# Kernel tuning notes

Hardware: AMD Instinct MI355X
Metric: run time of the kernel (lower is better)

The kernel has to match this reference:

```python
import jax, jax.numpy as jnp
import numpy as np

NEG_SLOPE = 0.2
N_NODES = 50000
N_EDGES = 800000
IN_DIM = 256
HID_DIM = 256
HEADS = 8
HEAD_DIM = HID_DIM // HEADS


def setup_inputs() -> dict:
    key = jax.random.key(0)
    ks = jax.random.split(key, 12)
    def glorot(k, shape):
        fan = sum(shape[-2:]) if len(shape) > 1 else shape[-1] + 1
        return jax.random.normal(k, shape, jnp.float32) * jnp.sqrt(2.0 / fan)
    return {
        "data": jax.random.normal(ks[0], (N_NODES, IN_DIM), jnp.float32),
        "src": jax.random.randint(ks[1], (N_EDGES,), 0, N_NODES),
        "dst": jax.random.randint(ks[2], (N_EDGES,), 0, N_NODES),
        "W1": glorot(ks[3], (IN_DIM, HID_DIM)),
        "al1": glorot(ks[4], (HEADS, HEAD_DIM)),
        "ar1": glorot(ks[5], (HEADS, HEAD_DIM)),
        "b1": jnp.zeros((HID_DIM,), jnp.float32),
        "W2": glorot(ks[6], (HID_DIM, HID_DIM)),
        "al2": glorot(ks[7], (HEADS, HEAD_DIM)),
        "ar2": glorot(ks[8], (HEADS, HEAD_DIM)),
        "b2": jnp.zeros((HID_DIM,), jnp.float32),
    }


def gat_layer(x, src, dst, W, al, ar, b):
    """One DGL-style GATConv layer with ReLU activation."""
    N = x.shape[0]
    feat = (x @ W).reshape(N, HEADS, HEAD_DIM)            # [N,H,D]
    el = jnp.sum(feat * al[None], axis=-1)                # [N,H]
    er = jnp.sum(feat * ar[None], axis=-1)                # [N,H]
    e = el[src] + er[dst]                                  # [E,H]
    e = jnp.where(e > 0, e, NEG_SLOPE * e)                 # LeakyReLU(0.2)
    # segment softmax over incoming edges of each dst node
    m = jax.ops.segment_max(e, dst, num_segments=N)        # [N,H] (-inf for empty)
    a = jnp.exp(e - m[dst])                                # [E,H]
    denom = jax.ops.segment_sum(a, dst, num_segments=N)    # [N,H]
    alpha = a / denom[dst]                                 # [E,H]
    msg = feat[src] * alpha[:, :, None]                    # [E,H,D]
    out = jax.ops.segment_sum(msg, dst, num_segments=N)    # [N,H,D]
    out = out + b.reshape(1, HEADS, HEAD_DIM)
    out = jax.nn.relu(out)
    return out.reshape(N, HID_DIM)


def reference(data, src, dst, W1, al1, ar1, b1, W2, al2, ar2, b2):
    h = gat_layer(data, src, dst, W1, al1, ar1, b1)
    h = gat_layer(h, src, dst, W2, al2, ar2, b2)
    return h
```

## Files before the change

### kernel.cpp

```cpp
#include <hip/hip_runtime.h>

#define N_NODES 50000
#define N_EDGES 800000
#define DIM 256
#define HEADS 8
#define NEG_SLOPE 0.2f

typedef unsigned short u16;
typedef float floatx4 __attribute__((ext_vector_type(4)));
typedef __bf16 bf16x8 __attribute__((ext_vector_type(8)));

__device__ __forceinline__ float b2f(u16 u) {
    union { unsigned int i; float f; } v; v.i = ((unsigned int)u) << 16; return v.f;
}
__device__ __forceinline__ u16 f2b(float f) {
    union { float f; unsigned int i; } v; v.f = f;
    unsigned int x = v.i;
    if ((x & 0x7f800000u) == 0x7f800000u && (x & 0x007fffffu)) {
        return (u16)((x >> 16) | 0x0040u);
    }
    unsigned int r = (x + 0x7fffu + ((x >> 16) & 1u)) >> 16;
    return (u16)r;
}

__global__ __launch_bounds__(256) void fill_u32(unsigned int* __restrict__ p,
                                                unsigned int v, int n) {
    int i = blockIdx.x * 256 + threadIdx.x;
    if (i < n) p[i] = v;
}

__global__ __launch_bounds__(256) void init_kernel(const unsigned int* __restrict__ d,
                                                   int* __restrict__ counts,
                                                   int* __restrict__ flag) {
    int i = blockIdx.x * 256 + threadIdx.x;
    if (i < N_NODES) counts[i] = 0;
    if (blockIdx.x == 0) {
        __shared__ int cnt;
        if (threadIdx.x == 0) cnt = 0;
        __syncthreads();
        unsigned int w = d[threadIdx.x];
        int bad = 0;
        #pragma unroll
        for (int half = 0; half < 2; ++half) {
            u16 u = (u16)(w >> (16 * half));
            unsigned int e = (u >> 7) & 0xFFu;
            if (u != 0 && (e >= 141u || e <= 27u)) bad = 1;
        }
        atomicAdd(&cnt, bad);
        __syncthreads();
        if (threadIdx.x == 0) *flag = (cnt > 64) ? 1 : 0;
    }
}

__global__ __launch_bounds__(256) void prep_kernel(const void* __restrict__ W1,
                                                   const void* __restrict__ W2,
                                                   u16* __restrict__ Wt1,
                                                   u16* __restrict__ Wt2,
                                                   const int* __restrict__ flagp) {
    const int isf = *flagp;
    int b = blockIdx.x;
    const void* W = (b < 16) ? W1 : W2;
    u16* Wt = (b < 16) ? Wt1 : Wt2;
    int t = b & 15;
    int k0 = (t >> 2) * 64, n0 = (t & 3) * 64;
    __shared__ float lt[64][65];
    int c = threadIdx.x & 63, r0 = threadIdx.x >> 6;
    #pragma unroll
    for (int j = 0; j < 16; ++j) {
        int r = j * 4 + r0;
        lt[r][c] = isf ? ((const float*)W)[(k0 + r) * 256 + n0 + c]
                       : b2f(((const u16*)W)[(k0 + r) * 256 + n0 + c]);
    }
    __syncthreads();
    #pragma unroll
    for (int j = 0; j < 16; ++j) {
        int rn = j * 4 + r0;
        Wt[(n0 + rn) * 256 + k0 + c] = f2b(lt[c][rn]);
    }
}

__global__ __launch_bounds__(256) void hist_kernel(const int* __restrict__ dst,
                                                   int* __restrict__ counts, int E) {
    int i = blockIdx.x * 256 + threadIdx.x;
    if (i < E) atomicAdd(&counts[dst[i]], 1);
}

__global__ __launch_bounds__(256) void scan_partial(const int* __restrict__ counts,
                                                    int* __restrict__ partial, int n) {
    int b = blockIdx.x, tid = threadIdx.x;
    int base = b * 1024 + tid * 4;
    int s = 0;
    #pragma unroll
    for (int k = 0; k < 4; ++k) if (base + k < n) s += counts[base + k];
    int lane = tid & 63;
    #pragma unroll
    for (int off = 32; off; off >>= 1) s += __shfl_xor(s, off);
    __shared__ int wsum[4];
    if (lane == 0) wsum[tid >> 6] = s;
    __syncthreads();
    if (tid == 0) partial[b] = wsum[0] + wsum[1] + wsum[2] + wsum[3];
}

__global__ __launch_bounds__(64) void scan_offsets(const int* __restrict__ partial,
                                                   int* __restrict__ offsets,
                                                   int* __restrict__ row_ptr,
                                                   int nb, int n) {
    int t = threadIdx.x;
    int v0 = (t < nb) ? partial[t] : 0;
    int v = v0;
    #pragma unroll
    for (int d = 1; d < 64; d <<= 1) {
        int u = __shfl_up(v, d);
        if (t >= d) v += u;
    }
    if (t < nb) offsets[t] = v - v0;
    if (t == 63) row_ptr[n] = v;
}

__global__ __launch_bounds__(256) void scan_write(const int* __restrict__ counts,
                                                  const int* __restrict__ offsets,
                                                  int* __restrict__ row_ptr,
                                                  int* __restrict__ wptr, int n) {
    int b = blockIdx.x, tid = threadIdx.x;
    int base = b * 1024 + tid * 4;
    int v[4]; int s = 0;
    #pragma unroll
    for (int k = 0; k < 4; ++k) { v[k] = (base + k < n) ? counts[base + k] : 0; s += v[k]; }
    int lane = tid & 63, w = tid >> 6;
    int incl = s;
    #pragma unroll
    for (int d = 1; d < 64; d <<= 1) {
        int u = __shfl_up(incl, d);
        if (lane >= d) incl += u;
    }
    __shared__ int wsum[4];
    if (lane == 63) wsum[w] = incl;
    __syncthreads();
    int woff = 0;
    for (int i = 0; i < w; ++i) woff += wsum[i];
    int run = offsets[b] + woff + incl - s;
    #pragma unroll
    for (int k = 0; k < 4; ++k) {
        if (base + k < n) { row_ptr[base + k] = run; wptr[base + k] = run; run += v[k]; }
    }
}

__global__ __launch_bounds__(256) void scatter_kernel(const int* __restrict__ src,
                                                      const int* __restrict__ dst,
                                                      int* __restrict__ wptr,
                                                      int* __restrict__ src_sorted, int E) {
    int i = blockIdx.x * 256 + threadIdx.x;
    if (i < E) {
        int pos = atomicAdd(&wptr[dst[i]], 1);
        src_sorted[pos] = src[i];
    }
}

#define LDA 264

__global__ __launch_bounds__(256, 3) void gemm_fused(const void* __restrict__ Araw,
                                                     int maybe_f32,
                                                     const u16* __restrict__ Wt,
                                                     u16* __restrict__ outF,
                                                     float* __restrict__ el,
                                                     float* __restrict__ er,
                                                     const void* __restrict__ al,
                                                     const void* __restrict__ ar,
                                                     int M, const int* __restrict__ flagp) {
    const int isf = *flagp;
    const bool af32 = (maybe_f32 != 0) && (isf != 0);
    __shared__ u16 As[64][LDA];
    const int tid  = threadIdx.x;
    const int w    = tid >> 6;
    const int lane = tid & 63;
    const int quad = lane >> 4;
    const int l16  = lane & 15;
    const int m0   = blockIdx.x * 64;

    const u16* wbase = Wt + (size_t)(64 * w + l16) * 256 + quad * 8;

    bf16x8 bCur[4], bNxt[4], aCur[4], aNxt[4];
    #pragma unroll
    for (int t = 0; t < 4; ++t)
        bCur[t] = *(const bf16x8*)(wbase + (size_t)t * 16 * 256);

    if (af32) {
        const float* Af = (const float*)Araw;
        #pragma unroll
        for (int it = 0; it < 8; ++it) {
            int idx = it * 256 + tid;
            int r = idx >> 5;
            int c = (idx & 31) << 3;
            int gr = m0 + r;
            u16 tb[8];
            if (gr < M) {
                float4 f0 = *(const float4*)(Af + (size_t)gr * 256 + c);
                float4 f1 = *(const float4*)(Af + (size_t)gr * 256 + c + 4);
                tb[0] = f2b(f0.x); tb[1] = f2b(f0.y); tb[2] = f2b(f0.z); tb[3] = f2b(f0.w);
                tb[4] = f2b(f1.x); tb[5] = f2b(f1.y); tb[6] = f2b(f1.z); tb[7] = f2b(f1.w);
            } else {
                #pragma unroll
                for (int k = 0; k < 8; ++k) tb[k] = 0;
            }
            *(uint4*)&As[r][c] = *(uint4*)tb;
        }
    } else {
        const u16* Ab = (const u16*)Araw;
        #pragma unroll
        for (int it = 0; it < 8; ++it) {
            int idx = it * 256 + tid;
            int r = idx >> 5;
            int c = (idx & 31) << 3;
            int gr = m0 + r;
            if (gr < M) {
                *(uint4*)&As[r][c] = *(const uint4*)(Ab + (size_t)gr * 256 + c);
            } else {
                uint4 z = {0u, 0u, 0u, 0u};
                *(uint4*)&As[r][c] = z;
            }
        }
    }
    __syncthreads();

    #pragma unroll
    for (int i = 0; i < 4; ++i)
        aCur[i] = *(const bf16x8*)&As[16 * i + l16][quad * 8];

    floatx4 acc[4][4] = {};

    #pragma unroll
    for (int s = 0; s < 8; ++s) {
        if (s < 7) {
            #pragma unroll
            for (int t = 0; t < 4; ++t)
                bNxt[t] = *(const bf16x8*)(wbase + (size_t)t * 16 * 256 + (s + 1) * 32);
            #pragma unroll
            for (int i = 0; i < 4; ++i)
                aNxt[i] = *(const bf16x8*)&As[16 * i + l16][(s + 1) * 32 + quad * 8];
        }
        #pragma unroll
        for (int i = 0; i < 4; ++i)
            #pragma unroll
            for (int t = 0; t < 4; ++t)
                acc[i][t] = __builtin_amdgcn_mfma_f32_16x16x32_bf16(aCur[i], bCur[t], acc[i][t], 0, 0, 0);
        if (s < 7) {
            #pragma unroll
            for (int t = 0; t < 4; ++t) bCur[t] = bNxt[t];
            #pragma unroll
            for (int i = 0; i < 4; ++i) aCur[i] = aNxt[i];
        }
    }

    #pragma unroll
    for (int i = 0; i < 4; ++i)
        #pragma unroll
        for (int t = 0; t < 4; ++t)
            #pragma unroll
            for (int r = 0; r < 4; ++r) {
                int row = m0 + 16 * i + quad * 4 + r;
                if (row < M) outF[(size_t)row * 256 + 64 * w + 16 * t + l16] = f2b(acc[i][t][r]);
            }

    float alv[4], arv[4];
    #pragma unroll
    for (int t = 0; t < 4; ++t) {
        int c = 64 * w + 16 * t + l16;
        alv[t] = isf ? ((const float*)al)[c] : b2f(((const u16*)al)[c]);
        arv[t] = isf ? ((const float*)ar)[c] : b2f(((const u16*)ar)[c]);
    }
    #pragma unroll
    for (int i = 0; i < 4; ++i)
        #pragma unroll
        for (int r = 0; r < 4; ++r) {
            int row = m0 + 16 * i + quad * 4 + r;
            #pragma unroll
            for (int tt = 0; tt < 2; ++tt) {
                float pl = acc[i][2 * tt][r] * alv[2 * tt] + acc[i][2 * tt + 1][r] * alv[2 * tt + 1];
                float pr = acc[i][2 * tt][r] * arv[2 * tt] + acc[i][2 * tt + 1][r] * arv[2 * tt + 1];
                #pragma unroll
                for (int mask = 1; mask <= 8; mask <<= 1) {
                    pl += __shfl_xor(pl, mask);
                    pr += __shfl_xor(pr, mask);
                }
                if (l16 == 0 && row < M) {
                    el[row * 8 + 2 * w + tt] = pl;
                    er[row * 8 + 2 * w + tt] = pr;
                }
            }
        }
}

__global__ __launch_bounds__(256) void aggregate_kernel(const u16* __restrict__ feat,
                                                        const float* __restrict__ el,
                                                        const float* __restrict__ er,
                                                        const void* __restrict__ bias,
                                                        const int* __restrict__ row_ptr,
                                                        const int* __restrict__ src_sorted,
                                                        void* __restrict__ out,
                                                        int out_mode,
                                                        int node0,
                                                        const int* __restrict__ flagp) {
    const int isf = *flagp;
    const int lane = threadIdx.x & 63;
    const int node = node0 + blockIdx.x * 4 + (threadIdx.x >> 6);
    if (node >= N_NODES) return;
    const int h = lane >> 3;
    const int j = lane & 7;
    const int beg = row_ptr[node];
    const int deg = row_ptr[node + 1] - beg;
    const float ern = er[node * HEADS + h];

    float m0v = -1e30f, ss0 = 0.f;
    float m1v = -1e30f, ss1 = 0.f;
    for (int i = j; i < deg; i += 16) {
        int s0 = src_sorted[beg + i];
        int i2 = i + 8;
        int s1 = (i2 < deg) ? src_sorted[beg + i2] : 0;
        float e0 = el[s0 * 8 + h] + ern;
        float e1 = el[s1 * 8 + h] + ern;
        e0 = e0 > 0.f ? e0 : NEG_SLOPE * e0;
        e1 = e1 > 0.f ? e1 : NEG_SLOPE * e1;
        if (i2 >= deg) e1 = -3e30f;
        float mn0 = fmaxf(m0v, e0);
        ss0 = ss0 * __expf(m0v - mn0) + __expf(e0 - mn0);
        m0v = mn0;
        float mn1 = fmaxf(m1v, e1);
        ss1 = ss1 * __expf(m1v - mn1) + __expf(e1 - mn1);
        m1v = mn1;
    }
    float m = fmaxf(m0v, m1v);
    float ssum = ss0 * __expf(m0v - m) + ss1 * __expf(m1v - m);
    #pragma unroll
    for (int mask = 1; mask <= 4; mask <<= 1) {
        float mo = __shfl_xor(m, mask);
        float so = __shfl_xor(ssum, mask);
        float mn = fmaxf(m, mo);
        ssum = ssum * __expf(m - mn) + so * __expf(mo - mn);
        m = mn;
    }
    const float mx = m;
    const float inv = ssum > 0.f ? 1.f / ssum : 0.f;

    const int q = lane & 31;
    const int half = lane >> 5;
    const int hq = q >> 2;
    float a[8] = {};

    int sC = 0; float avC = 0.f;
    if (j < deg) {
        sC = src_sorted[beg + j];
        float e = el[sC * 8 + h] + ern;
        e = e > 0.f ? e : NEG_SLOPE * e;
        avC = __expf(e - mx) * inv;
    }
    uint4 f[4]; float ae[4];
    #pragma unroll
    for (int u = 0; u < 4; ++u) {
        int sel = hq * 8 + 2 * u + half;
        int se = __shfl(sC, sel);
        ae[u] = __shfl(avC, sel);
        f[u] = *(const uint4*)(feat + (size_t)se * DIM + 8 * q);
    }

    #pragma unroll 2
    for (int c0 = 0; c0 < deg; c0 += 8) {
        uint4 f2[4]; float ae2[4];
        {
            int sN = 0; float avN = 0.f;
            int i = c0 + 8 + j;
            if (i < deg) {
                sN = src_sorted[beg + i];
                float e = el[sN * 8 + h] + ern;
                e = e > 0.f ? e : NEG_SLOPE * e;
                avN = __expf(e - mx) * inv;
            }
            #pragma unroll
            for (int u = 0; u < 4; ++u) {
                int sel = hq * 8 + 2 * u + half;
                int se = __shfl(sN, sel);
                ae2[u] = __shfl(avN, sel);
                f2[u] = *(const uint4*)(feat + (size_t)se * DIM + 8 * q);
            }
        }
        #pragma unroll
        for (int u = 0; u < 4; ++u) {
            float wgt = ae[u];
            a[0] += wgt * b2f((u16)(f[u].x & 0xffffu)); a[1] += wgt * b2f((u16)(f[u].x >> 16));
            a[2] += wgt * b2f((u16)(f[u].y & 0xffffu)); a[3] += wgt * b2f((u16)(f[u].y >> 16));
            a[4] += wgt * b2f((u16)(f[u].z & 0xffffu)); a[5] += wgt * b2f((u16)(f[u].z >> 16));
            a[6] += wgt * b2f((u16)(f[u].w & 0xffffu)); a[7] += wgt * b2f((u16)(f[u].w >> 16));
        }
        #pragma unroll
        for (int u = 0; u < 4; ++u) { f[u] = f2[u]; ae[u] = ae2[u]; }
    }

    #pragma unroll
    for (int k = 0; k < 8; ++k) a[k] += __shfl_xor(a[k], 32);

    if (half == 0) {
        float o[8];
        if (isf) {
            float4 b0 = *(const float4*)((const float*)bias + 8 * q);
            float4 b1 = *(const float4*)((const float*)bias + 8 * q + 4);
            o[0] = a[0] + b0.x; o[1] = a[1] + b0.y; o[2] = a[2] + b0.z; o[3] = a[3] + b0.w;
            o[4] = a[4] + b1.x; o[5] = a[5] + b1.y; o[6] = a[6] + b1.z; o[7] = a[7] + b1.w;
        } else {
            uint4 bu = *(const uint4*)((const u16*)bias + 8 * q);
            o[0] = a[0] + b2f((u16)(bu.x & 0xffffu)); o[1] = a[1] + b2f((u16)(bu.x >> 16));
            o[2] = a[2] + b2f((u16)(bu.y & 0xffffu)); o[3] = a[3] + b2f((u16)(bu.y >> 16));
            o[4] = a[4] + b2f((u16)(bu.z & 0xffffu)); o[5] = a[5] + b2f((u16)(bu.z >> 16));
            o[6] = a[6] + b2f((u16)(bu.w & 0xffffu)); o[7] = a[7] + b2f((u16)(bu.w >> 16));
        }
        #pragma unroll
        for (int k = 0; k < 8; ++k) o[k] = fmaxf(o[k], 0.f);
        if (out_mode == 0 || !isf) {
            u16 pk[8] = {f2b(o[0]), f2b(o[1]), f2b(o[2]), f2b(o[3]),
                         f2b(o[4]), f2b(o[5]), f2b(o[6]), f2b(o[7])};
            *(uint4*)((u16*)out + (size_t)node * DIM + 8 * q) = *(uint4*)pk;
        } else {
            float4 v0 = {o[0], o[1], o[2], o[3]};
            float4 v1 = {o[4], o[5], o[6], o[7]};
            *(float4*)((float*)out + (size_t)node * DIM + 8 * q) = v0;
            *(float4*)((float*)out + (size_t)node * DIM + 8 * q + 4) = v1;
        }
    }
}

extern "C" void kernel_launch(void* const* d_in, const int* in_sizes, int n_in,
                              void* d_out, int out_size, void* d_ws, size_t ws_size,
                              hipStream_t stream) {
    const void* data = d_in[0];
    const int* src = (const int*)d_in[1];
    const int* dst = (const int*)d_in[2];
    const void* W1  = d_in[3];
    const void* al1 = d_in[4];
    const void* ar1 = d_in[5];
    const void* b1  = d_in[6];
    const void* W2  = d_in[7];
    const void* al2 = d_in[8];
    const void* ar2 = d_in[9];
    const void* b2  = d_in[10];

    const size_t NEEDED =
        (size_t)N_NODES * DIM * 2 +
        (size_t)N_NODES * HEADS * 4 * 2 +
        (size_t)N_NODES * 4 * 2 +
        (size_t)(N_NODES + 4) * 4 +
        (size_t)N_EDGES * 4 +
        2 * 256 * 256 * 2 +
        1024;

    if (ws_size < NEEDED) {
        int nwords = (out_size + 1) / 2;
        fill_u32<<<(nwords + 255) / 256, 256, 0, stream>>>(
            (unsigned int*)d_out, 0x42C842C8u, nwords);
        return;
    }

    char* ws = (char*)d_ws;
    u16* feat = (u16*)ws;        ws += (size_t)N_NODES * DIM * 2;
    float* el = (float*)ws;      ws += (size_t)N_NODES * HEADS * 4;
    float* er = (float*)ws;      ws += (size_t)N_NODES * HEADS * 4;
    int* counts = (int*)ws;      ws += (size_t)N_NODES * 4;
    int* wptr = (int*)ws;        ws += (size_t)N_NODES * 4;
    int* row_ptr = (int*)ws;     ws += (size_t)(N_NODES + 4) * 4;
    int* src_sorted = (int*)ws;  ws += (size_t)N_EDGES * 4;
    u16* Wt1 = (u16*)ws;         ws += 256 * 256 * 2;
    u16* Wt2 = (u16*)ws;         ws += 256 * 256 * 2;
    int* partial = (int*)ws;     ws += 256;
    int* offsets = (int*)ws;     ws += 256;
    int* flag = (int*)ws;        ws += 256;

    u16* h1 = (u16*)d_out;

    const int nb = (N_NODES + 1023) / 1024;

    init_kernel<<<(N_NODES + 255) / 256, 256, 0, stream>>>(
        (const unsigned int*)data, counts, flag);
    prep_kernel<<<32, 256, 0, stream>>>(W1, W2, Wt1, Wt2, flag);
    hist_kernel<<<(N_EDGES + 255) / 256, 256, 0, stream>>>(dst, counts, N_EDGES);
    scan_partial<<<nb, 256, 0, stream>>>(counts, partial, N_NODES);
    scan_offsets<<<1, 64, 0, stream>>>(partial, offsets, row_ptr, nb, N_NODES);
    scan_write<<<nb, 256, 0, stream>>>(counts, offsets, row_ptr, wptr, N_NODES);
    scatter_kernel<<<(N_EDGES + 255) / 256, 256, 0, stream>>>(src, dst, wptr, src_sorted, N_EDGES);

    const int gemm_blocks = (N_NODES + 63) / 64;
    const int HALF = 25000;
    const int agg_half_blocks = HALF / 4;

    gemm_fused<<<gemm_blocks, 256, 0, stream>>>(data, 1, Wt1, feat,
                                                el, er, al1, ar1, N_NODES, flag);
    aggregate_kernel<<<agg_half_blocks, 256, 0, stream>>>(feat, el, er, b1, row_ptr, src_sorted,
                                                          (void*)h1, 0, 0, flag);
    aggregate_kernel<<<agg_half_blocks, 256, 0, stream>>>(feat, el, er, b1, row_ptr, src_sorted,
                                                          (void*)h1, 0, HALF, flag);
    gemm_fused<<<gemm_blocks, 256, 0, stream>>>(h1, 0, Wt2, feat,
                                                el, er, al2, ar2, N_NODES, flag);
    aggregate_kernel<<<agg_half_blocks, 256, 0, stream>>>(feat, el, er, b2, row_ptr, src_sorted,
                                                          d_out, 2, 0, flag);
    aggregate_kernel<<<agg_half_blocks, 256, 0, stream>>>(feat, el, er, b2, row_ptr, src_sorted,
                                                          d_out, 2, HALF, flag);
}
```

Before: 426.8 us.

## Replace CSR build with padded per-node adjacency and stage GEMM output via LDS

Replaces the histogram/scan/scatter CSR construction with a single atomic build kernel that writes each edge into a fixed MAXDEG=64 slot per destination node, sending overflow edges to a global list. The aggregate kernels scan that list only for nodes whose degree exceeds the cap. The GEMM epilogue now stages bf16 results through shared memory so it can issue coalesced 16-byte row stores. This removes four small launches and the scan passes, at the cost of a larger workspace and a slow path for high-degree nodes.

New measurement: 394.4 us. -7.6%, faster.

```diff
diff --git a/kernel.cpp b/kernel.cpp
--- a/kernel.cpp
+++ b/kernel.cpp
@@ -5,6 +5,8 @@
 #define DIM 256
 #define HEADS 8
 #define NEG_SLOPE 0.2f
+#define MAXDEG 64
+#define OVFCAP 65536
 
 typedef unsigned short u16;
 typedef float floatx4 __attribute__((ext_vector_type(4)));
@@ -31,12 +33,13 @@
 
 __global__ __launch_bounds__(256) void init_kernel(const unsigned int* __restrict__ d,
                                                    int* __restrict__ counts,
-                                                   int* __restrict__ flag) {
+                                                   int* __restrict__ flag,
+                                                   int* __restrict__ novf) {
     int i = blockIdx.x * 256 + threadIdx.x;
     if (i < N_NODES) counts[i] = 0;
     if (blockIdx.x == 0) {
         __shared__ int cnt;
-        if (threadIdx.x == 0) cnt = 0;
+        if (threadIdx.x == 0) { cnt = 0; *novf = 0; }
         __syncthreads();
         unsigned int w = d[threadIdx.x];
         int bad = 0;
@@ -76,6 +79,26 @@
     for (int j = 0; j < 16; ++j) {
         int rn = j * 4 + r0;
         Wt[(n0 + rn) * 256 + k0 + c] = f2b(lt[c][rn]);
+    }
+}
+
+__global__ __launch_bounds__(256) void build_kernel(const int* __restrict__ src,
+                                                    const int* __restrict__ dst,
+                                                    int* __restrict__ counts,
+                                                    int* __restrict__ padded,
+                                                    int* __restrict__ novf,
+                                                    int2* __restrict__ ovf, int E) {
+    int i = blockIdx.x * 256 + threadIdx.x;
+    if (i < E) {
+        int d = dst[i];
+        int s = src[i];
+        int pos = atomicAdd(&counts[d], 1);
+        if (pos < MAXDEG) {
+            padded[d * MAXDEG + pos] = s;
+        } else {
+            int oi = atomicAdd(novf, 1);
+            if (oi < OVFCAP) { int2 pr; pr.x = d; pr.y = s; ovf[oi] = pr; }
+        }
     }
 }
 
@@ -251,15 +274,31 @@
         }
     }
 
+    __syncthreads();
+    u16* Ct = (u16*)As;
     #pragma unroll
     for (int i = 0; i < 4; ++i)
         #pragma unroll
-        for (int t = 0; t < 4; ++t)
-            #pragma unroll
-            for (int r = 0; r < 4; ++r) {
-                int row = m0 + 16 * i + quad * 4 + r;
-                if (row < M) outF[(size_t)row * 256 + 64 * w + 16 * t + l16] = f2b(acc[i][t][r]);
-            }
+        for (int t = 0; t < 4; ++t) {
+            int col = 64 * w + 16 * t + l16;
+            #pragma unroll
+            for (int r = 0; r < 4; ++r)
+                Ct[(16 * i + quad * 4 + r) * LDA + col] = f2b(acc[i][t][r]);
+        }
+    __syncthreads();
+    #pragma unroll
+    for (int it = 0; it < 4; ++it) {
+        int idx = it * 256 + tid;
+        int row = idx >> 4;
+        int c16 = (idx & 15) * 16;
+        int gr = m0 + row;
+        if (gr < M) {
+            uint4 v0 = *(const uint4*)&Ct[row * LDA + c16];
+            uint4 v1 = *(const uint4*)&Ct[row * LDA + c16 + 8];
+            *(uint4*)(outF + (size_t)gr * 256 + c16) = v0;
+            *(uint4*)(outF + (size_t)gr * 256 + c16 + 8) = v1;
+        }
+    }
 
     float alv[4], arv[4];
     #pragma unroll
@@ -294,33 +333,40 @@
                                                         const float* __restrict__ el,
                                                         const float* __restrict__ er,
                                                         const void* __restrict__ bias,
-                                                        const int* __restrict__ row_ptr,
-                                                        const int* __restrict__ src_sorted,
+                                                        const int* __restrict__ idxinfo,
+                                                        const int* __restrict__ srcbuf,
                                                         void* __restrict__ out,
                                                         int out_mode,
                                                         int node0,
-                                                        const int* __restrict__ flagp) {
+                                                        const int* __restrict__ flagp,
+                                                        int pmode,
+                                                        const int* __restrict__ novfp,
+                                                        const int2* __restrict__ ovf) {
     const int isf = *flagp;
     const int lane = threadIdx.x & 63;
     const int node = node0 + blockIdx.x * 4 + (threadIdx.x >> 6);
     if (node >= N_NODES) return;
     const int h = lane >> 3;
     const int j = lane & 7;
-    const int beg = row_ptr[node];
-    const int deg = row_ptr[node + 1] - beg;
+    int beg, deg;
+    if (pmode) { beg = node * MAXDEG; deg = idxinfo[node]; }
+    else       { beg = idxinfo[node]; deg = idxinfo[node + 1] - beg; }
+    const int dcap = (pmode && deg > MAXDEG) ? MAXDEG : deg;
+    int nov = 0;
+    if (pmode && deg > MAXDEG) { nov = *novfp; if (nov > OVFCAP) nov = OVFCAP; }
     const float ern = er[node * HEADS + h];
 
     float m0v = -1e30f, ss0 = 0.f;
     float m1v = -1e30f, ss1 = 0.f;
-    for (int i = j; i < deg; i += 16) {
-        int s0 = src_sorted[beg + i];
+    for (int i = j; i < dcap; i += 16) {
+        int s0 = srcbuf[beg + i];
         int i2 = i + 8;
-        int s1 = (i2 < deg) ? src_sorted[beg + i2] : 0;
+        int s1 = (i2 < dcap) ? srcbuf[beg + i2] : 0;
         float e0 = el[s0 * 8 + h] + ern;
         float e1 = el[s1 * 8 + h] + ern;
         e0 = e0 > 0.f ? e0 : NEG_SLOPE * e0;
         e1 = e1 > 0.f ? e1 : NEG_SLOPE * e1;
-        if (i2 >= deg) e1 = -3e30f;
+        if (i2 >= dcap) e1 = -3e30f;
         float mn0 = fmaxf(m0v, e0);
         ss0 = ss0 * __expf(m0v - mn0) + __expf(e0 - mn0);
         m0v = mn0;
@@ -328,6 +374,15 @@
         ss1 = ss1 * __expf(m1v - mn1) + __expf(e1 - mn1);
         m1v = mn1;
     }
+    for (int k = j; k < nov; k += 8) {
+        int2 pr = ovf[k];
+        if (pr.x != node) continue;
+        float e = el[pr.y * 8 + h] + ern;
+        e = e > 0.f ? e : NEG_SLOPE * e;
+        float mn = fmaxf(m0v, e);
+        ss0 = ss0 * __expf(m0v - mn) + __expf(e - mn);
+        m0v = mn;
+    }
     float m = fmaxf(m0v, m1v);
     float ssum = ss0 * __expf(m0v - m) + ss1 * __expf(m1v - m);
     #pragma unroll
@@ -347,8 +402,8 @@
     float a[8] = {};
 
     int sC = 0; float avC = 0.f;
-    if (j < deg) {
-        sC = src_sorted[beg + j];
+    if (j < dcap) {
+        sC = srcbuf[beg + j];
         float e = el[sC * 8 + h] + ern;
         e = e > 0.f ? e : NEG_SLOPE * e;
         avC = __expf(e - mx) * inv;
@@ -363,13 +418,13 @@
     }
 
     #pragma unroll 2
-    for (int c0 = 0; c0 < deg; c0 += 8) {
+    for (int c0 = 0; c0 < dcap; c0 += 8) {
         uint4 f2[4]; float ae2[4];
         {
             int sN = 0; float avN = 0.f;
             int i = c0 + 8 + j;
-            if (i < deg) {
-                sN = src_sorted[beg + i];
+            if (i < dcap) {
+                sN = srcbuf[beg + i];
                 float e = el[sN * 8 + h] + ern;
                 e = e > 0.f ? e : NEG_SLOPE * e;
                 avN = __expf(e - mx) * inv;
@@ -392,6 +447,27 @@
         }
         #pragma unroll
         for (int u = 0; u < 4; ++u) { f[u] = f2[u]; ae[u] = ae2[u]; }
+    }
+
+    if (nov) {
+        const float mxq  = __shfl(mx, hq * 8);
+        const float invq = __shfl(inv, hq * 8);
+        const float ernq = __shfl(ern, hq * 8);
+        for (int k = 0; k < nov; ++k) {
+            int2 pr = ovf[k];
+            if (pr.x != node) continue;
+            float av = 0.f;
+            if (half == 0) {
+                float e = el[pr.y * 8 + hq] + ernq;
+                e = e > 0.f ? e : NEG_SLOPE * e;
+                av = __expf(e - mxq) * invq;
+            }
+            uint4 fv = *(const uint4*)(feat + (size_t)pr.y * DIM + 8 * q);
+            a[0] += av * b2f((u16)(fv.x & 0xffffu)); a[1] += av * b2f((u16)(fv.x >> 16));
+            a[2] += av * b2f((u16)(fv.y & 0xffffu)); a[3] += av * b2f((u16)(fv.y >> 16));
+            a[4] += av * b2f((u16)(fv.z & 0xffffu)); a[5] += av * b2f((u16)(fv.z >> 16));
+            a[6] += av * b2f((u16)(fv.w & 0xffffu)); a[7] += av * b2f((u16)(fv.w >> 16));
+        }
     }
 
     #pragma unroll
@@ -441,16 +517,18 @@
     const void* ar2 = d_in[9];
     const void* b2  = d_in[10];
 
-    const size_t NEEDED =
+    const size_t BASE =
         (size_t)N_NODES * DIM * 2 +
         (size_t)N_NODES * HEADS * 4 * 2 +
-        (size_t)N_NODES * 4 * 2 +
-        (size_t)(N_NODES + 4) * 4 +
-        (size_t)N_EDGES * 4 +
+        (size_t)N_NODES * 4 +
         2 * 256 * 256 * 2 +
         1024;
-
-    if (ws_size < NEEDED) {
+    const size_t NEEDED_PAD = BASE + (size_t)N_NODES * MAXDEG * 4 + (size_t)OVFCAP * 8;
+    const size_t NEEDED_CSR = BASE + (size_t)N_NODES * 4 +
+                              (size_t)(N_NODES + 4) * 4 +
+                              (size_t)N_EDGES * 4;
+
+    if (ws_size < NEEDED_CSR && ws_size < NEEDED_PAD) {
         int nwords = (out_size + 1) / 2;
         fill_u32<<<(nwords + 255) / 256, 256, 0, stream>>>(
             (unsigned int*)d_out, 0x42C842C8u, nwords);
@@ -462,42 +540,56 @@
     float* el = (float*)ws;      ws += (size_t)N_NODES * HEADS * 4;
     float* er = (float*)ws;      ws += (size_t)N_NODES * HEADS * 4;
     int* counts = (int*)ws;      ws += (size_t)N_NODES * 4;
-    int* wptr = (int*)ws;        ws += (size_t)N_NODES * 4;
-    int* row_ptr = (int*)ws;     ws += (size_t)(N_NODES + 4) * 4;
-    int* src_sorted = (int*)ws;  ws += (size_t)N_EDGES * 4;
     u16* Wt1 = (u16*)ws;         ws += 256 * 256 * 2;
     u16* Wt2 = (u16*)ws;         ws += 256 * 256 * 2;
+    int* flag = (int*)ws;        ws += 256;
+    int* novf = (int*)ws;        ws += 256;
     int* partial = (int*)ws;     ws += 256;
     int* offsets = (int*)ws;     ws += 256;
-    int* flag = (int*)ws;        ws += 256;
 
     u16* h1 = (u16*)d_out;
-
-    const int nb = (N_NODES + 1023) / 1024;
-
-    init_kernel<<<(N_NODES + 255) / 256, 256, 0, stream>>>(
-        (const unsigned int*)data, counts, flag);
-    prep_kernel<<<32, 256, 0, stream>>>(W1, W2, Wt1, Wt2, flag);
-    hist_kernel<<<(N_EDGES + 255) / 256, 256, 0, stream>>>(dst, counts, N_EDGES);
-    scan_partial<<<nb, 256, 0, stream>>>(counts, partial, N_NODES);
-    scan_offsets<<<1, 64, 0, stream>>>(partial, offsets, row_ptr, nb, N_NODES);
-    scan_write<<<nb, 256, 0, stream>>>(counts, offsets, row_ptr, wptr, N_NODES);
-    scatter_kernel<<<(N_EDGES + 255) / 256, 256, 0, stream>>>(src, dst, wptr, src_sorted, N_EDGES);
-
     const int gemm_blocks = (N_NODES + 63) / 64;
     const int HALF = 25000;
     const int agg_half_blocks = HALF / 4;
 
+    init_kernel<<<(N_NODES + 255) / 256, 256, 0, stream>>>(
+        (const unsigned int*)data, counts, flag, novf);
+    prep_kernel<<<32, 256, 0, stream>>>(W1, W2, Wt1, Wt2, flag);
+
+    const int* idxinfo;
+    const int* srcbuf;
+    const int2* ovf = (const int2*)d_ws;
+    int pmode;
+
+    if (ws_size >= NEEDED_PAD) {
+        int* padded = (int*)ws;  ws += (size_t)N_NODES * MAXDEG * 4;
+        int2* ovfw = (int2*)ws;  ws += (size_t)OVFCAP * 8;
+        build_kernel<<<(N_EDGES + 255) / 256, 256, 0, stream>>>(
+            src, dst, counts, padded, novf, ovfw, N_EDGES);
+        idxinfo = counts; srcbuf = padded; ovf = ovfw; pmode = 1;
+    } else {
+        int* wptr = (int*)ws;        ws += (size_t)N_NODES * 4;
+        int* row_ptr = (int*)ws;     ws += (size_t)(N_NODES + 4) * 4;
+        int* src_sorted = (int*)ws;  ws += (size_t)N_EDGES * 4;
+        const int nb = (N_NODES + 1023) / 1024;
+        hist_kernel<<<(N_EDGES + 255) / 256, 256, 0, stream>>>(dst, counts, N_EDGES);
+        scan_partial<<<nb, 256, 0, stream>>>(counts, partial, N_NODES);
+        scan_offsets<<<1, 64, 0, stream>>>(partial, offsets, row_ptr, nb, N_NODES);
+        scan_write<<<nb, 256, 0, stream>>>(counts, offsets, row_ptr, wptr, N_NODES);
+        scatter_kernel<<<(N_EDGES + 255) / 256, 256, 0, stream>>>(src, dst, wptr, src_sorted, N_EDGES);
+        idxinfo = row_ptr; srcbuf = src_sorted; pmode = 0;
+    }
+
     gemm_fused<<<gemm_blocks, 256, 0, stream>>>(data, 1, Wt1, feat,
                                                 el, er, al1, ar1, N_NODES, flag);
-    aggregate_kernel<<<agg_half_blocks, 256, 0, stream>>>(feat, el, er, b1, row_ptr, src_sorted,
-                                                          (void*)h1, 0, 0, flag);
-    aggregate_kernel<<<agg_half_blocks, 256, 0, stream>>>(feat, el, er, b1, row_ptr, src_sorted,
-                                                          (void*)h1, 0, HALF, flag);
+    aggregate_kernel<<<agg_half_blocks, 256, 0, stream>>>(feat, el, er, b1, idxinfo, srcbuf,
+                                                          (void*)h1, 0, 0, flag, pmode, novf, ovf);
+    aggregate_kernel<<<agg_half_blocks, 256, 0, stream>>>(feat, el, er, b1, idxinfo, srcbuf,
+                                                          (void*)h1, 0, HALF, flag, pmode, novf, ovf);
     gemm_fused<<<gemm_blocks, 256, 0, stream>>>(h1, 0, Wt2, feat,
                                                 el, er, al2, ar2, N_NODES, flag);
-    aggregate_kernel<<<agg_half_blocks, 256, 0, stream>>>(feat, el, er, b2, row_ptr, src_sorted,
-                                                          d_out, 2, 0, flag);
-    aggregate_kernel<<<agg_half_blocks, 256, 0, stream>>>(feat, el, er, b2, row_ptr, src_sorted,
-                                                          d_out, 2, HALF, flag);
-}
+    aggregate_kernel<<<agg_half_blocks, 256, 0, stream>>>(feat, el, er, b2, idxinfo, srcbuf,
+                                                          d_out, 2, 0, flag, pmode, novf, ovf);
+    aggregate_kernel<<<agg_half_blocks, 256, 0, stream>>>(feat, el, er, b2, idxinfo, srcbuf,
+                                                          d_out, 2, HALF, flag, pmode, novf, ovf);
+}
```
